# Kernel tuning notes

Hardware: AMD Instinct MI355X
Metric: run time of the kernel (lower is better)

The kernel has to match this reference:

```python
import jax, jax.numpy as jnp
import numpy as np


def _operators_3_to_2(x2d, A, norm):
    # x2d: [b, d, n, n], A: [b, n, n]. Returns the 20 basis tensors, each [b, d, n, n].
    t = lambda a: a.transpose(0, 1, 3, 2)
    shape = x2d.shape
    op1 = jnp.einsum('bdij,bij,bik->bdjk', x2d, A, A) / norm
    op2 = jnp.einsum('bdij,bij,bjk->bdik', x2d, A, A) / norm
    op3 = jnp.einsum('bdij,bik,bjk->bdij', x2d, A, A) / norm
    op4 = jnp.broadcast_to(jnp.einsum('bdij,bij->bdi', x2d, A)[..., None], shape) / norm
    op5 = jnp.broadcast_to(jnp.einsum('bdij,bij->bdj', x2d, A)[..., None], shape) / norm
    op6 = jnp.einsum('bdij,bik->bdjk', x2d, A) / norm
    # NOTE: source has ops7 = [op6, op6.transpose] (bug: op7 computed but unused) -- replicated faithfully.
    op8 = jnp.einsum('bdij,bik->bdij', x2d, A) / norm
    op9 = jnp.einsum('bdij,bjk->bdij', x2d, A) / norm
    op10 = jnp.broadcast_to(x2d.sum(3, keepdims=True), shape) / norm
    op11 = jnp.broadcast_to(x2d.sum(2, keepdims=True), shape) / norm
    return [op1, t(op1), op2, t(op2), op3,
            op4, t(op4), op5, t(op5),
            op6, t(op6), op6, t(op6),
            op8, op9,
            op10, t(op10), op11, t(op11),
            x2d]


def _forward(x, edge_weight, coeffs1, bias1, coeffs2, bias2, edge_index, batch, n):
    f = x.shape[-1]
    b = x.shape[0] // n
    # to_2d_tensor: [b*n, f] -> [b, 2f, n, n]
    x2 = x.reshape(b, n, f).transpose(0, 2, 1)  # [b, f, n]
    x_2d = jnp.concatenate([
        jnp.broadcast_to(x2[:, :, :, None], (b, f, n, n)),
        jnp.broadcast_to(x2[:, :, None, :], (b, f, n, n)),
    ], axis=1)
    # to_dense_adj: scatter-add edge weights into per-graph dense [b, n, n]
    g = batch[edge_index[0]]
    r = edge_index[0] - g * n
    c = edge_index[1] - g * n
    A = jnp.zeros((b, n, n), x.dtype).at[g, r, c].add(edge_weight)
    norm = jnp.asarray(n, x.dtype)  # normalization=True default
    for li, (coeffs, bias) in enumerate([(coeffs1, bias1), (coeffs2, bias2)]):
        ops_out = jnp.stack(_operators_3_to_2(x_2d, A, norm), axis=2)  # [b, d, 20, n, n]
        x_2d = jnp.einsum('der,bdrij->beij', coeffs, ops_out) + bias
        if li == 0:
            x_2d = jax.nn.sigmoid(x_2d)
    return x_2d.mean(axis=(1, 2, 3))  # [b]


def setup_inputs() -> dict:
    key = jax.random.key(0)
    kx, kg, ks, kd, kw, kc1, kc2 = jax.random.split(key, 7)
    b, n, deg, f, h = 4, 128, 16, 32, 32
    d_in, d_out = 2 * f, 2 * h  # layer doubles channels; hidden layer is d_out -> d_out
    E = b * n * deg
    x = jax.random.normal(kx, (b * n, f), dtype=jnp.float32)
    g = jax.random.randint(kg, (E,), 0, b)
    src = jax.random.randint(ks, (E,), 0, n)
    dst = jax.random.randint(kd, (E,), 0, n)
    edge_index = jnp.stack([g * n + src, g * n + dst]).astype(jnp.int32)
    edge_weight = jax.random.uniform(kw, (E,), dtype=jnp.float32)
    batch = (jnp.arange(b * n) // n).astype(jnp.int32)
    scale1 = np.sqrt(2.0) / (d_in + d_out)
    scale2 = np.sqrt(2.0) / (d_out + d_out)
    coeffs1 = jax.random.normal(kc1, (d_in, d_out, 20), dtype=jnp.float32) * scale1
    coeffs2 = jax.random.normal(kc2, (d_out, d_out, 20), dtype=jnp.float32) * scale2
    bias1 = jnp.zeros((1, d_out, 1, 1), dtype=jnp.float32)
    bias2 = jnp.zeros((1, d_out, 1, 1), dtype=jnp.float32)
    return {"x": x, "edge_weight": edge_weight, "coeffs1": coeffs1, "bias1": bias1,
            "coeffs2": coeffs2, "bias2": bias2, "edge_index": edge_index,
            "batch": batch, "n": n}


def reference(x, edge_weight, coeffs1, bias1, coeffs2, bias2, edge_index, batch, n):
    return _forward(x, edge_weight, coeffs1, bias1, coeffs2, bias2, edge_index, batch, n)
```

## Files before the change

kernel.cpp:

```cpp
#include <hip/hip_runtime.h>
#include <stdint.h>

typedef unsigned short u16;
using short8 = __attribute__((ext_vector_type(8))) short;
using f32x4  = __attribute__((ext_vector_type(4))) float;

#define NB 4
#define NN 128
#define NF 32
#define ND 64
#define NMAT (NB*ND*NN*NN)

#define OFF_A     0u
#define OFF_ACC   262144u
#define OFF_AAT   262400u
#define OFF_RA    524544u
#define OFF_W     526592u
#define OFF_RM    1116416u
#define OFF_CM    1247488u
#define OFF_RX    1378560u
#define OFF_CX    1509632u
#define OFF_BF    1640960u
#define OFF_ATB   1641472u
#define OFF_WB    1772544u
#define OFF_X2    1936384u
#define OFF_XE    10324992u
#define OFF_UA    18713600u
#define OFF_UB    27102208u
#define OFF_UC    35490816u
#define OFF_UD    43879424u
#define OFF_YACC  52268032u

__device__ __forceinline__ float b2f(u16 v){
  union { uint32_t u; float f; } x; x.u = ((uint32_t)v) << 16; return x.f;
}
__device__ __forceinline__ u16 f2b(float f){
  union { uint32_t u; float f2; } x; x.f2 = f;
  uint32_t u = x.u;
  return (u16)((u + 0x7FFFu + ((u >> 16) & 1u)) >> 16);
}

#define MFMA16(a,b,c) __builtin_amdgcn_mfma_f32_16x16x32_bf16((a),(b),(c),0,0,0)

__device__ __constant__ signed char dR1[18] = {0,9,1,10,2,3,4,13,14,19,5,7,15,18,6,8,16,17};
__device__ __constant__ signed char dR2[18] = {-1,11,-1,12,-1,-1,-1,-1,-1,-1,-1,-1,-1,-1,-1,-1,-1,-1};

__global__ void k_setup(const int* __restrict__ ei, const int* __restrict__ bat,
                        const void* __restrict__ ews, float* __restrict__ A, int E,
                        const void* __restrict__ xs, u16* __restrict__ Xe,
                        const void* __restrict__ c1s, const void* __restrict__ c2s,
                        const void* __restrict__ b1s, const void* __restrict__ b2s,
                        float* __restrict__ W, u16* __restrict__ Wb,
                        float* __restrict__ bfv)
{
  __shared__ int flg;
  const u16* x16 = (const u16*)xs;
  if (threadIdx.x == 0) flg = 0;
  __syncthreads();
  int hit = 0;
  for (int k = threadIdx.x; k < 1024; k += 256){
    u16 u = x16[k];
    if (((u >> 7) & 0xFF) >= 0x90) hit = 1;
  }
  if (hit) flg = 1;
  __syncthreads();
  const int isf = flg;

  const int bx = blockIdx.x;
  if (bx < 32){
    if (bx == 0 && threadIdx.x < 128){
      int tt = threadIdx.x;
      const void* bsrc = (tt < 64) ? b1s : b2s;
      int idx = tt & 63;
      bfv[tt] = isf ? ((const float*)bsrc)[idx] : b2f(((const u16*)bsrc)[idx]);
    }
    for (int t = bx*256 + threadIdx.x; t < E; t += 32*256){
      int s = ei[t], dnode = ei[E + t];
      int g = bat[s];
      int r = s - g*NN, c = dnode - g*NN;
      float wv = isf ? ((const float*)ews)[t] : b2f(((const u16*)ews)[t]);
      atomicAdd(&A[(g*NN + r)*NN + c], wv);
    }
  } else if (bx < 32 + 2048){
    int gid = (bx - 32)*256 + threadIdx.x;
    int ij8 = gid & 2047;
    int d   = (gid >> 11) & 63;
    int b   = gid >> 17;
    int ij  = ij8*8;
    int i = ij >> 7, j0 = ij & 127;
    short8 v;
    if (d < NF){
      int idx = (b*NN + i)*NF + d;
      u16 bv = isf ? f2b(((const float*)xs)[idx]) : ((const u16*)xs)[idx];
      #pragma unroll
      for (int k = 0; k < 8; k++) v[k] = (short)bv;
    } else {
      int dd = d - NF;
      #pragma unroll
      for (int k = 0; k < 8; k++){
        int idx = (b*NN + j0 + k)*NF + dd;
        v[k] = (short)(isf ? f2b(((const float*)xs)[idx]) : ((const u16*)xs)[idx]);
      }
    }
    *(short8*)(Xe + ((size_t)(b*ND + d) << 14) + ij) = v;
  } else {
    int gl = (bx - 2080)*256 + threadIdx.x;
    if (gl >= 2*1152*64) return;
    int L = gl / (1152*64);
    int rem = gl - L*1152*64;
    int row = rem >> 6, e = rem & 63;
    int slot = row >> 6, d = row & 63;
    const void* cr = L ? c2s : c1s;
    int base = (d*64 + e)*20;
    int i1 = base + dR1[slot];
    float v = isf ? ((const float*)cr)[i1] : b2f(((const u16*)cr)[i1]);
    if (dR2[slot] >= 0){
      int i2 = base + dR2[slot];
      v += isf ? ((const float*)cr)[i2] : b2f(((const u16*)cr)[i2]);
    }
    float scale = (slot == 9) ? 1.0f : (1.0f/128.0f);
    v *= scale;
    W[gl] = v;
    if (slot < 10)
      Wb[(((size_t)L*10 + slot)*64 + e)*64 + d] = f2b(v);
  }
}

__global__ __launch_bounds__(256) void k_prepA(const float* __restrict__ A, float* __restrict__ AAt,
                                               u16* __restrict__ ATb, float* __restrict__ rA){
  const int iq = blockIdx.x, b = blockIdx.y;
  const int t = threadIdx.x;
  if (iq < 8){
    int j = t & 127, ih = t >> 7;
    const float* Ab = A + b*NN*NN;
    float acc[8] = {0,0,0,0,0,0,0,0};
    for (int k = 0; k < NN; k++){
      float aj = Ab[j*NN + k];
      #pragma unroll
      for (int ii = 0; ii < 8; ii++){
        int i = iq*16 + ih*8 + ii;
        acc[ii] += Ab[i*NN + k] * aj;
      }
    }
    #pragma unroll
    for (int ii = 0; ii < 8; ii++){
      int i = iq*16 + ih*8 + ii;
      AAt[(b*NN + i)*NN + j] = acc[ii];
    }
  } else if (iq == 8){
    __shared__ float lds[128][129];
    for (int l = 0; l < 64; l++){
      int idx = l*256 + t;
      lds[idx >> 7][idx & 127] = A[b*16384 + idx];
    }
    __syncthreads();
    for (int l = 0; l < 64; l++){
      int idx = l*256 + t;
      int r = idx >> 7, c = idx & 127;
      ATb[b*16384 + idx] = f2b(lds[c][r]);
    }
  } else {
    if (t < 128){
      const float* Ab = A + (b*NN + t)*NN;
      float s = 0.f;
      for (int j = 0; j < 128; j++) s += Ab[j];
      rA[b*NN + t] = s;
    }
  }
}

#define SJ32 70
#define SJF  67
#define SXE  34

__global__ __launch_bounds__(256) void k_mixrow(const u16* __restrict__ Xe, const float* __restrict__ A,
    const float* __restrict__ AAt, const float* __restrict__ rA, const u16* __restrict__ Wb,
    u16* __restrict__ Ua, u16* __restrict__ Ub, u16* __restrict__ Uc, u16* __restrict__ Ud,
    float* __restrict__ Yacc,
    float* __restrict__ RM, float* __restrict__ CM,
    float* __restrict__ RX, float* __restrict__ CXv)
{
  const int b = blockIdx.y;
  const int t = threadIdx.x;

  if (blockIdx.x >= 256){
    const int d = blockIdx.x - 256;
    const u16* Xd = Xe + ((size_t)(b*ND + d) << 14);
    const float* Ab = A + b*NN*NN;
    float sm = 0.f, sx = 0.f;
    if (t < 128){
      const int i = t;
      #pragma unroll 2
      for (int j8 = 0; j8 < 16; j8++){
        short8 xv = *(const short8*)(Xd + i*128 + j8*8);
        float4 a0 = *(const float4*)(Ab + i*128 + j8*8);
        float4 a1 = *(const float4*)(Ab + i*128 + j8*8 + 4);
        float x0 = b2f((u16)xv[0]), x1 = b2f((u16)xv[1]), x2 = b2f((u16)xv[2]), x3 = b2f((u16)xv[3]);
        float x4 = b2f((u16)xv[4]), x5 = b2f((u16)xv[5]), x6 = b2f((u16)xv[6]), x7 = b2f((u16)xv[7]);
        sx += x0+x1+x2+x3+x4+x5+x6+x7;
        sm += x0*a0.x + x1*a0.y + x2*a0.z + x3*a0.w
            + x4*a1.x + x5*a1.y + x6*a1.z + x7*a1.w;
      }
      RM[(b*64 + d)*128 + i] = sm;
      RX[(b*64 + d)*128 + i] = sx;
    } else {
      const int j = t - 128;
      for (int i = 0; i < 128; i++){
        float xv = b2f(Xd[i*128 + j]);
        sx += xv;
        sm += xv * Ab[i*128 + j];
      }
      CM[(b*64 + d)*128 + j] = sm;
      CXv[(b*64 + d)*128 + j] = sx;
    }
    return;
  }

  const int w = t >> 6, lane = t & 63;
  const int col = lane & 15, quad = lane >> 4;
  const int ij0 = blockIdx.x*64;

  __shared__ uint32_t lsb[4][32*SJ32];
  __shared__ float lsf[64*SJF];

  short8 wa[10][2];
  #pragma unroll
  for (int s = 0; s < 10; s++){
    const u16* wp = Wb + (size_t)((s*64 + w*16 + col)*64 + quad*8);
    wa[s][0] = *(const short8*)wp;
    wa[s][1] = *(const short8*)(wp + 32);
  }
  float a_s[4], t_s[4], rjv[4];
  #pragma unroll
  for (int sj = 0; sj < 4; sj++){
    int ij = ij0 + sj*16 + col;
    a_s[sj] = A[b*16384 + ij];
    t_s[sj] = AAt[b*16384 + ij];
    rjv[sj] = rA[b*128 + (ij & 127)];
  }
  const float riv = rA[b*128 + (ij0 >> 7)];

  uint32_t* ldsX = &lsb[0][0];
  {
    const int ep = t >> 3;
    const int s8 = (t & 7)*8;
    const u16* xp = Xe + ((size_t)(b*ND + 2*ep) << 14) + ij0 + s8;
    short8 r0 = *(const short8*)xp;
    short8 r1 = *(const short8*)(xp + 16384);
    #pragma unroll
    for (int k = 0; k < 8; k++)
      ldsX[(s8 + k)*SXE + ep] = ((uint32_t)(u16)r0[k]) | (((uint32_t)(u16)r1[k]) << 16);
  }
  __syncthreads();
  short8 xb[4][2];
  #pragma unroll
  for (int sj = 0; sj < 4; sj++){
    #pragma unroll
    for (int h = 0; h < 2; h++){
      const uint32_t* p = &ldsX[(sj*16 + col)*SXE + quad*4 + h*16];
      uint2 u0 = *(const uint2*)p;
      uint2 u1 = *(const uint2*)(p + 2);
      union { uint32_t u[4]; short8 s; } cv;
      cv.u[0] = u0.x; cv.u[1] = u0.y; cv.u[2] = u1.x; cv.u[3] = u1.y;
      xb[sj][h] = cv.s;
    }
  }
  __syncthreads();

  #pragma unroll
  for (int g = 0; g < 5; g++){
    const int s0_tab[5]  = {0, 2, 4, 5, 6};
    const int nsl_tab[5] = {2, 2, 1, 1, 4};
    const int s0 = s0_tab[g], nsl = nsl_tab[g];
    #pragma unroll
    for (int sj = 0; sj < 4; sj++){
      f32x4 acc[4];
      #pragma unroll
      for (int s = 0; s < 4; s++) acc[s] = (f32x4){0.f,0.f,0.f,0.f};
      #pragma unroll
      for (int s = 0; s < 4; s++){
        if (s >= nsl) break;
        acc[s] = MFMA16(wa[s0+s][0], xb[sj][0], acc[s]);
        acc[s] = MFMA16(wa[s0+s][1], xb[sj][1], acc[s]);
      }
      if (g < 4){
        float v[4];
        #pragma unroll
        for (int r = 0; r < 4; r++){
          if (g == 2 || g == 3) v[r] = acc[0][r]*a_s[sj];
          else                  v[r] = acc[0][r]*a_s[sj] + acc[1][r];
        }
        uint32_t p0 = (uint32_t)f2b(v[0]) | ((uint32_t)f2b(v[1]) << 16);
        uint32_t p1 = (uint32_t)f2b(v[2]) | ((uint32_t)f2b(v[3]) << 16);
        int ep = w*8 + quad*2;
        lsb[g][ep*SJ32 + sj*16 + col] = p0;
        lsb[g][(ep + 1)*SJ32 + sj*16 + col] = p1;
      } else {
        #pragma unroll
        for (int r = 0; r < 4; r++){
          float v = acc[0][r]*t_s[sj] + acc[1][r]*riv + acc[2][r]*rjv[sj] + acc[3][r];
          lsf[(w*16 + quad*4 + r)*SJF + sj*16 + col] = v;
        }
      }
    }
  }
  __syncthreads();

  const int eo = t >> 2, seg = t & 3;
  const int ep = eo >> 1, sh = (eo & 1)*16;
  #pragma unroll
  for (int g = 0; g < 4; g++){
    const uint32_t* lp = &lsb[g][ep*SJ32 + seg*16];
    short8 v0, v1;
    #pragma unroll
    for (int k = 0; k < 8; k++){
      v0[k] = (short)((lp[k]   >> sh) & 0xffffu);
      v1[k] = (short)((lp[8+k] >> sh) & 0xffffu);
    }
    u16* U = (g==0)?Ua:(g==1)?Ub:(g==2)?Uc:Ud;
    u16* dst = U + ((size_t)(b*64 + eo) << 14) + ij0 + seg*16;
    *(short8*)dst = v0;
    *(short8*)(dst + 8) = v1;
  }
  {
    const float* fp = &lsf[eo*SJF + seg*16];
    float* dst = Yacc + ((size_t)(b*64 + eo) << 14) + ij0 + seg*16;
    #pragma unroll
    for (int q = 0; q < 4; q++)
      *(float4*)(dst + q*4) = make_float4(fp[q*4], fp[q*4+1], fp[q*4+2], fp[q*4+3]);
  }
}

#define SLT 68

__global__ __launch_bounds__(256) void k_tne(const u16* __restrict__ ATb,
    const u16* __restrict__ Ua, const u16* __restrict__ Ub,
    const u16* __restrict__ Uc, const u16* __restrict__ Ud,
    const float* __restrict__ Yacc, const float* __restrict__ W,
    const float* __restrict__ RM, const float* __restrict__ CM,
    const float* __restrict__ RX, const float* __restrict__ CXv,
    const float* __restrict__ bias, u16* __restrict__ Xout, float* __restrict__ acc4, int last)
{
  const int nh = blockIdx.x, be = blockIdx.y;
  const int b = be >> 6, e = be & 63;
  const int t = threadIdx.x, wave = t >> 6, lane = t & 63;
  const int col = lane & 15, quad = lane >> 4;
  const int m0 = (wave >> 1)*64;
  const int n0 = nh*64 + (wave & 1)*32;
  const int nb0 = nh*64;

  __shared__ uint32_t uls[128*SLT];
  __shared__ uint32_t ubl[64*SLT];
  __shared__ float radd[128], cadd[128];
  __shared__ float red[4];

  if (t < 128){
    int i = t; float s = 0.f;
    for (int d = 0; d < ND; d++){
      int v = (b*ND + d)*NN + i;
      s += W[(640 + d)*64 + e]*RM[v] + W[(704 + d)*64 + e]*CM[v]
         + W[(768 + d)*64 + e]*RX[v] + W[(832 + d)*64 + e]*CXv[v];
    }
    radd[i] = s;
  } else {
    int j = t - 128; float s = 0.f;
    for (int d = 0; d < ND; d++){
      int v = (b*ND + d)*NN + j;
      s += W[(896 + d)*64 + e]*RM[v] + W[(960 + d)*64 + e]*CM[v]
         + W[(1024 + d)*64 + e]*RX[v] + W[(1088 + d)*64 + e]*CXv[v];
    }
    cadd[j] = s;
  }

  const u16* ua = Ua + ((size_t)be << 14);
  const u16* ub = Ub + ((size_t)be << 14);
  {
    const int kp = t >> 2;
    #pragma unroll
    for (int it = 0; it < 4; it++){
      int mo = it*4 + (t & 3);
      short8 r0 = *(const short8*)(ua + (2*kp)*128 + mo*8);
      short8 r1 = *(const short8*)(ua + (2*kp + 1)*128 + mo*8);
      #pragma unroll
      for (int x = 0; x < 8; x++)
        uls[(mo*8 + x)*SLT + kp] = ((uint32_t)(u16)r0[x]) | (((uint32_t)(u16)r1[x]) << 16);
    }
    #pragma unroll
    for (int it = 0; it < 2; it++){
      int no = it*4 + (t & 3);
      short8 r0 = *(const short8*)(ub + (2*kp)*128 + nb0 + no*8);
      short8 r1 = *(const short8*)(ub + (2*kp + 1)*128 + nb0 + no*8);
      #pragma unroll
      for (int x = 0; x < 8; x++)
        ubl[(no*8 + x)*SLT + kp] = ((uint32_t)(u16)r0[x]) | (((uint32_t)(u16)r1[x]) << 16);
    }
  }
  __syncthreads();

  f32x4 acc[4][2];
  #pragma unroll
  for (int mt = 0; mt < 4; mt++)
    #pragma unroll
    for (int nt = 0; nt < 2; nt++)
      acc[mt][nt] = (f32x4){0.f,0.f,0.f,0.f};

  const u16* at = ATb + ((size_t)b << 14);
  short8 at_n[4][2];
  #pragma unroll
  for (int kq = 0; kq < 4; kq++){
    int k0 = kq*32 + quad*8;
    at_n[kq][0] = *(const short8*)(at + (n0 + col)*128 + k0);
    at_n[kq][1] = *(const short8*)(at + (n0 + 16 + col)*128 + k0);
  }

  #pragma unroll
  for (int kq = 0; kq < 4; kq++){
    int kd = kq*16 + quad*4;
    #pragma unroll
    for (int mt = 0; mt < 4; mt++){
      short8 af = *(const short8*)&uls[(m0 + mt*16 + col)*SLT + kd];
      acc[mt][0] = MFMA16(af, at_n[kq][0], acc[mt][0]);
      acc[mt][1] = MFMA16(af, at_n[kq][1], acc[mt][1]);
    }
  }
  #pragma unroll
  for (int kq = 0; kq < 4; kq++){
    int k0 = kq*32 + quad*8, kd = kq*16 + quad*4;
    short8 bf0 = *(const short8*)&ubl[((wave & 1)*32 + 0*16 + col)*SLT + kd];
    short8 bf1 = *(const short8*)&ubl[((wave & 1)*32 + 1*16 + col)*SLT + kd];
    #pragma unroll
    for (int mt = 0; mt < 4; mt++){
      short8 af = *(const short8*)(at + (m0 + mt*16 + col)*128 + k0);
      acc[mt][0] = MFMA16(af, bf0, acc[mt][0]);
      acc[mt][1] = MFMA16(af, bf1, acc[mt][1]);
    }
  }
  {
    const u16* uc = Uc + ((size_t)be << 14);
    #pragma unroll
    for (int kq = 0; kq < 4; kq++){
      int k0 = kq*32 + quad*8;
      #pragma unroll
      for (int mt = 0; mt < 4; mt++){
        short8 af = *(const short8*)(uc + (m0 + mt*16 + col)*128 + k0);
        acc[mt][0] = MFMA16(af, at_n[kq][0], acc[mt][0]);
        acc[mt][1] = MFMA16(af, at_n[kq][1], acc[mt][1]);
      }
    }
  }
  {
    const u16* ud = Ud + ((size_t)be << 14);
    #pragma unroll
    for (int kq = 0; kq < 4; kq++){
      int k0 = kq*32 + quad*8;
      short8 bf0 = *(const short8*)(ud + (n0 + col)*128 + k0);
      short8 bf1 = *(const short8*)(ud + (n0 + 16 + col)*128 + k0);
      #pragma unroll
      for (int mt = 0; mt < 4; mt++){
        short8 af = *(const short8*)(at + (m0 + mt*16 + col)*128 + k0);
        acc[mt][0] = MFMA16(af, bf0, acc[mt][0]);
        acc[mt][1] = MFMA16(af, bf1, acc[mt][1]);
      }
    }
  }
  __syncthreads();

  uint32_t* stg = uls;
  const float bv = bias[e];
  const float* Y = Yacc + ((size_t)be << 14);
  if (!last){
    #pragma unroll
    for (int mt = 0; mt < 4; mt++)
      #pragma unroll
      for (int nt = 0; nt < 2; nt++)
        #pragma unroll
        for (int rp = 0; rp < 2; rp++){
          uint32_t p = 0;
          #pragma unroll
          for (int h = 0; h < 2; h++){
            int r = rp*2 + h;
            int row = m0 + mt*16 + quad*4 + r;
            int cn = n0 + nt*16 + col;
            float v = acc[mt][nt][r] + Y[row*128 + cn] + radd[row] + cadd[cn] + bv;
            v = 1.f/(1.f + __expf(-v));
            p |= ((uint32_t)f2b(v)) << (16*h);
          }
          int ipair = (m0 + mt*16 + quad*4) >> 1;
          stg[(ipair + rp)*SLT + (wave & 1)*32 + nt*16 + col] = p;
        }
    __syncthreads();
    const uint32_t* lp = &stg[(t >> 2)*SLT + (t & 1)*32];
    const int sh = ((t >> 1) & 1)*16;
    u16* dst = Xout + ((size_t)be << 14) + (size_t)(t >> 1)*128 + nh*64 + (t & 1)*32;
    #pragma unroll
    for (int q2 = 0; q2 < 4; q2++){
      short8 v;
      #pragma unroll
      for (int k = 0; k < 8; k++) v[k] = (short)((lp[q2*8 + k] >> sh) & 0xffffu);
      *(short8*)(dst + q2*8) = v;
    }
  } else {
    float loc = 0.f;
    #pragma unroll
    for (int mt = 0; mt < 4; mt++)
      #pragma unroll
      for (int nt = 0; nt < 2; nt++)
        #pragma unroll
        for (int r = 0; r < 4; r++){
          int row = m0 + mt*16 + quad*4 + r;
          int cn = n0 + nt*16 + col;
          loc += acc[mt][nt][r] + Y[row*128 + cn] + radd[row] + cadd[cn] + bv;
        }
    for (int off = 32; off > 0; off >>= 1) loc += __shfl_down(loc, off, 64);
    if (lane == 0) red[wave] = loc;
    __syncthreads();
    if (t == 0) atomicAdd(&acc4[b], red[0] + red[1] + red[2] + red[3]);
  }
}

__global__ void k_finish(const float* __restrict__ acc4, const u16* __restrict__ x16,
                         void* __restrict__ out){
  __shared__ int flg;
  int t = threadIdx.x;
  if (t == 0) flg = 0;
  __syncthreads();
  int hit = 0;
  for (int k = t; k < 512; k += 64){
    u16 u = x16[k];
    if (((u >> 7) & 0xFF) >= 0x90) hit = 1;
  }
  if (hit) flg = 1;
  __syncthreads();
  if (t < NB){
    float v = acc4[t] * (1.0f/1048576.0f);
    if (flg) ((float*)out)[t] = v;
    else     ((u16*)out)[t] = f2b(v);
  }
}

extern "C" void kernel_launch(void* const* d_in, const int* in_sizes, int n_in,
                              void* d_out, int out_size, void* d_ws, size_t ws_size,
                              hipStream_t stream)
{
  const void* x   = d_in[0];
  const void* ew  = d_in[1];
  const void* c1  = d_in[2];
  const void* b1  = d_in[3];
  const void* c2  = d_in[4];
  const void* b2  = d_in[5];
  const int* ei  = (const int*)d_in[6];
  const int* bat = (const int*)d_in[7];
  const int E = in_sizes[1];

  char* wsb = (char*)d_ws;
  float* A    = (float*)(wsb + OFF_A);
  float* acc4 = (float*)(wsb + OFF_ACC);
  float* AAt  = (float*)(wsb + OFF_AAT);
  float* rA   = (float*)(wsb + OFF_RA);
  float* W    = (float*)(wsb + OFF_W);
  float* RM   = (float*)(wsb + OFF_RM);
  float* CM   = (float*)(wsb + OFF_CM);
  float* RX   = (float*)(wsb + OFF_RX);
  float* CXv  = (float*)(wsb + OFF_CX);
  float* bfv  = (float*)(wsb + OFF_BF);
  u16* ATb = (u16*)(wsb + OFF_ATB);
  u16* Wb  = (u16*)(wsb + OFF_WB);
  u16* X2  = (u16*)(wsb + OFF_X2);
  u16* Xe  = (u16*)(wsb + OFF_XE);
  u16* Ua  = (u16*)(wsb + OFF_UA);
  u16* Ub  = (u16*)(wsb + OFF_UB);
  u16* Uc  = (u16*)(wsb + OFF_UC);
  u16* Ud  = (u16*)(wsb + OFF_UD);
  float* Yacc = (float*)(wsb + OFF_YACC);

  hipMemsetAsync(wsb, 0, OFF_AAT, stream);

  k_setup<<<dim3(2656), dim3(256), 0, stream>>>(ei, bat, ew, A, E, x, Xe,
                                                c1, c2, b1, b2, W, Wb, bfv);
  k_prepA<<<dim3(10, NB), dim3(256), 0, stream>>>(A, AAt, ATb, rA);

  for (int L = 0; L < 2; L++){
    const float* Wl = W + (size_t)L*1152*64;
    const u16*  Wbl = Wb + (size_t)L*10*64*64;
    const u16*  Xsrc = (L == 0) ? Xe : X2;
    k_mixrow<<<dim3(320, NB), dim3(256), 0, stream>>>(Xsrc, A, AAt, rA, Wbl,
                                                      Ua, Ub, Uc, Ud, Yacc, RM, CM, RX, CXv);
    k_tne<<<dim3(2, 256), dim3(256), 0, stream>>>(ATb, Ua, Ub, Uc, Ud, Yacc, Wl,
                                                  RM, CM, RX, CXv, bfv + L*64, X2, acc4, L);
  }
  k_finish<<<dim3(1), dim3(64), 0, stream>>>(acc4, (const u16*)x, d_out);
}
```

Measured before the change: 223.0 us.

## Skip materializing expanded layer-0 input; read compact x directly in mixrow

Drops the 8 MB broadcast-expanded Xe tensor built in k_setup. Layer 0 of k_mixrow now reads a compact bf16 copy of x and builds the LDS tile from it. Its row and column reductions are computed analytically from x, row sums and new column sums of A. k_prepA is also rewritten to compute A·Aᵀ with more blocks and float4 loads, and to produce column sums from the LDS transpose tile. This removes a large write and re-read of redundant data, at the cost of a special-cased first-layer path with strided scalar loads.

```diff
diff --git a/kernel.cpp b/kernel.cpp
--- a/kernel.cpp
+++ b/kernel.cpp
@@ -24,7 +24,8 @@
 #define OFF_ATB   1641472u
 #define OFF_WB    1772544u
 #define OFF_X2    1936384u
-#define OFF_XE    10324992u
+#define OFF_XC    10324992u
+#define OFF_CA    10357760u
 #define OFF_UA    18713600u
 #define OFF_UB    27102208u
 #define OFF_UC    35490816u
@@ -47,7 +48,7 @@
 
 __global__ void k_setup(const int* __restrict__ ei, const int* __restrict__ bat,
                         const void* __restrict__ ews, float* __restrict__ A, int E,
-                        const void* __restrict__ xs, u16* __restrict__ Xe,
+                        const void* __restrict__ xs, u16* __restrict__ xc,
                         const void* __restrict__ c1s, const void* __restrict__ c2s,
                         const void* __restrict__ b1s, const void* __restrict__ b2s,
                         float* __restrict__ W, u16* __restrict__ Wb,
@@ -81,30 +82,19 @@
       float wv = isf ? ((const float*)ews)[t] : b2f(((const u16*)ews)[t]);
       atomicAdd(&A[(g*NN + r)*NN + c], wv);
     }
-  } else if (bx < 32 + 2048){
-    int gid = (bx - 32)*256 + threadIdx.x;
-    int ij8 = gid & 2047;
-    int d   = (gid >> 11) & 63;
-    int b   = gid >> 17;
-    int ij  = ij8*8;
-    int i = ij >> 7, j0 = ij & 127;
-    short8 v;
-    if (d < NF){
-      int idx = (b*NN + i)*NF + d;
-      u16 bv = isf ? f2b(((const float*)xs)[idx]) : ((const u16*)xs)[idx];
-      #pragma unroll
-      for (int k = 0; k < 8; k++) v[k] = (short)bv;
+  } else if (bx < 40){
+    int idx8 = ((bx - 32)*256 + threadIdx.x)*8;
+    if (!isf){
+      *(short8*)(xc + idx8) = *(const short8*)(x16 + idx8);
     } else {
-      int dd = d - NF;
-      #pragma unroll
-      for (int k = 0; k < 8; k++){
-        int idx = (b*NN + j0 + k)*NF + dd;
-        v[k] = (short)(isf ? f2b(((const float*)xs)[idx]) : ((const u16*)xs)[idx]);
-      }
-    }
-    *(short8*)(Xe + ((size_t)(b*ND + d) << 14) + ij) = v;
+      const float* xfp = (const float*)xs;
+      short8 v;
+      #pragma unroll
+      for (int k = 0; k < 8; k++) v[k] = (short)f2b(xfp[idx8 + k]);
+      *(short8*)(xc + idx8) = v;
+    }
   } else {
-    int gl = (bx - 2080)*256 + threadIdx.x;
+    int gl = (bx - 40)*256 + threadIdx.x;
     if (gl >= 2*1152*64) return;
     int L = gl / (1152*64);
     int rem = gl - L*1152*64;
@@ -127,27 +117,26 @@
 }
 
 __global__ __launch_bounds__(256) void k_prepA(const float* __restrict__ A, float* __restrict__ AAt,
-                                               u16* __restrict__ ATb, float* __restrict__ rA){
+                                               u16* __restrict__ ATb, float* __restrict__ rA,
+                                               float* __restrict__ cA){
   const int iq = blockIdx.x, b = blockIdx.y;
   const int t = threadIdx.x;
-  if (iq < 8){
+  if (iq < 32){
     int j = t & 127, ih = t >> 7;
+    int i0 = iq*4 + ih, i1 = i0 + 2;
     const float* Ab = A + b*NN*NN;
-    float acc[8] = {0,0,0,0,0,0,0,0};
-    for (int k = 0; k < NN; k++){
-      float aj = Ab[j*NN + k];
-      #pragma unroll
-      for (int ii = 0; ii < 8; ii++){
-        int i = iq*16 + ih*8 + ii;
-        acc[ii] += Ab[i*NN + k] * aj;
-      }
-    }
-    #pragma unroll
-    for (int ii = 0; ii < 8; ii++){
-      int i = iq*16 + ih*8 + ii;
-      AAt[(b*NN + i)*NN + j] = acc[ii];
-    }
-  } else if (iq == 8){
+    float acc0 = 0.f, acc1 = 0.f;
+    #pragma unroll 4
+    for (int k = 0; k < 128; k += 4){
+      float4 aj = *(const float4*)(Ab + j*128 + k);
+      float4 a0 = *(const float4*)(Ab + i0*128 + k);
+      float4 a1 = *(const float4*)(Ab + i1*128 + k);
+      acc0 += a0.x*aj.x + a0.y*aj.y + a0.z*aj.z + a0.w*aj.w;
+      acc1 += a1.x*aj.x + a1.y*aj.y + a1.z*aj.z + a1.w*aj.w;
+    }
+    AAt[(b*NN + i0)*NN + j] = acc0;
+    AAt[(b*NN + i1)*NN + j] = acc1;
+  } else {
     __shared__ float lds[128][129];
     for (int l = 0; l < 64; l++){
       int idx = l*256 + t;
@@ -159,12 +148,15 @@
       int r = idx >> 7, c = idx & 127;
       ATb[b*16384 + idx] = f2b(lds[c][r]);
     }
-  } else {
     if (t < 128){
-      const float* Ab = A + (b*NN + t)*NN;
       float s = 0.f;
-      for (int j = 0; j < 128; j++) s += Ab[j];
+      for (int j = 0; j < 128; j++) s += lds[t][j];
       rA[b*NN + t] = s;
+    } else {
+      int c = t - 128;
+      float s = 0.f;
+      for (int j = 0; j < 128; j++) s += lds[j][c];
+      cA[b*NN + c] = s;
     }
   }
 }
@@ -173,19 +165,58 @@
 #define SJF  67
 #define SXE  34
 
-__global__ __launch_bounds__(256) void k_mixrow(const u16* __restrict__ Xe, const float* __restrict__ A,
-    const float* __restrict__ AAt, const float* __restrict__ rA, const u16* __restrict__ Wb,
+__global__ __launch_bounds__(256) void k_mixrow(const u16* __restrict__ Xs, const float* __restrict__ A,
+    const float* __restrict__ AAt, const float* __restrict__ rA, const float* __restrict__ cA,
+    const u16* __restrict__ xc, const u16* __restrict__ Wb,
     u16* __restrict__ Ua, u16* __restrict__ Ub, u16* __restrict__ Uc, u16* __restrict__ Ud,
     float* __restrict__ Yacc,
     float* __restrict__ RM, float* __restrict__ CM,
-    float* __restrict__ RX, float* __restrict__ CXv)
+    float* __restrict__ RX, float* __restrict__ CXv, int first)
 {
   const int b = blockIdx.y;
   const int t = threadIdx.x;
 
   if (blockIdx.x >= 256){
     const int d = blockIdx.x - 256;
-    const u16* Xd = Xe + ((size_t)(b*ND + d) << 14);
+    if (first){
+      if (t < 128){
+        const int i = t;
+        if (d < NF){
+          float xv = b2f(xc[(b*NN + i)*NF + d]);
+          RM[(b*64 + d)*128 + i] = xv * rA[b*NN + i];
+          RX[(b*64 + d)*128 + i] = 128.f * xv;
+        } else {
+          const u16* xcb = xc + b*NN*NF + (d - NF);
+          const float* Ar = A + b*16384 + i*128;
+          float sm = 0.f, sx = 0.f;
+          for (int j = 0; j < 128; j++){
+            float xj = b2f(xcb[j*NF]);
+            sm += Ar[j]*xj; sx += xj;
+          }
+          RM[(b*64 + d)*128 + i] = sm;
+          RX[(b*64 + d)*128 + i] = sx;
+        }
+      } else {
+        const int j = t - 128;
+        if (d < NF){
+          const u16* xcb = xc + b*NN*NF + d;
+          const float* Ac = A + b*16384 + j;
+          float sm = 0.f, sx = 0.f;
+          for (int i = 0; i < 128; i++){
+            float xi = b2f(xcb[i*NF]);
+            sm += Ac[i*128]*xi; sx += xi;
+          }
+          CM[(b*64 + d)*128 + j] = sm;
+          CXv[(b*64 + d)*128 + j] = sx;
+        } else {
+          float xv = b2f(xc[(b*NN + j)*NF + (d - NF)]);
+          CM[(b*64 + d)*128 + j] = xv * cA[b*NN + j];
+          CXv[(b*64 + d)*128 + j] = 128.f * xv;
+        }
+      }
+      return;
+    }
+    const u16* Xd = Xs + ((size_t)(b*ND + d) << 14);
     const float* Ab = A + b*NN*NN;
     float sm = 0.f, sx = 0.f;
     if (t < 128){
@@ -244,12 +275,27 @@
   {
     const int ep = t >> 3;
     const int s8 = (t & 7)*8;
-    const u16* xp = Xe + ((size_t)(b*ND + 2*ep) << 14) + ij0 + s8;
-    short8 r0 = *(const short8*)xp;
-    short8 r1 = *(const short8*)(xp + 16384);
-    #pragma unroll
-    for (int k = 0; k < 8; k++)
-      ldsX[(s8 + k)*SXE + ep] = ((uint32_t)(u16)r0[k]) | (((uint32_t)(u16)r1[k]) << 16);
+    if (first){
+      const int i = ij0 >> 7;
+      const int j0 = (ij0 & 127) + s8;
+      if (ep < 16){
+        uint32_t p = *(const uint32_t*)(xc + (b*NN + i)*NF + 2*ep);
+        #pragma unroll
+        for (int k = 0; k < 8; k++) ldsX[(s8 + k)*SXE + ep] = p;
+      } else {
+        const int d0 = 2*ep - 32;
+        #pragma unroll
+        for (int k = 0; k < 8; k++)
+          ldsX[(s8 + k)*SXE + ep] = *(const uint32_t*)(xc + (b*NN + j0 + k)*NF + d0);
+      }
+    } else {
+      const u16* xp = Xs + ((size_t)(b*ND + 2*ep) << 14) + ij0 + s8;
+      short8 r0 = *(const short8*)xp;
+      short8 r1 = *(const short8*)(xp + 16384);
+      #pragma unroll
+      for (int k = 0; k < 8; k++)
+        ldsX[(s8 + k)*SXE + ep] = ((uint32_t)(u16)r0[k]) | (((uint32_t)(u16)r1[k]) << 16);
+    }
   }
   __syncthreads();
   short8 xb[4][2];
@@ -566,7 +612,8 @@
   u16* ATb = (u16*)(wsb + OFF_ATB);
   u16* Wb  = (u16*)(wsb + OFF_WB);
   u16* X2  = (u16*)(wsb + OFF_X2);
-  u16* Xe  = (u16*)(wsb + OFF_XE);
+  u16* xc  = (u16*)(wsb + OFF_XC);
+  float* cA = (float*)(wsb + OFF_CA);
   u16* Ua  = (u16*)(wsb + OFF_UA);
   u16* Ub  = (u16*)(wsb + OFF_UB);
   u16* Uc  = (u16*)(wsb + OFF_UC);
@@ -575,16 +622,16 @@
 
   hipMemsetAsync(wsb, 0, OFF_AAT, stream);
 
-  k_setup<<<dim3(2656), dim3(256), 0, stream>>>(ei, bat, ew, A, E, x, Xe,
-                                                c1, c2, b1, b2, W, Wb, bfv);
-  k_prepA<<<dim3(10, NB), dim3(256), 0, stream>>>(A, AAt, ATb, rA);
+  k_setup<<<dim3(616), dim3(256), 0, stream>>>(ei, bat, ew, A, E, x, xc,
+                                               c1, c2, b1, b2, W, Wb, bfv);
+  k_prepA<<<dim3(33, NB), dim3(256), 0, stream>>>(A, AAt, ATb, rA, cA);
 
   for (int L = 0; L < 2; L++){
     const float* Wl = W + (size_t)L*1152*64;
     const u16*  Wbl = Wb + (size_t)L*10*64*64;
-    const u16*  Xsrc = (L == 0) ? Xe : X2;
-    k_mixrow<<<dim3(320, NB), dim3(256), 0, stream>>>(Xsrc, A, AAt, rA, Wbl,
-                                                      Ua, Ub, Uc, Ud, Yacc, RM, CM, RX, CXv);
+    k_mixrow<<<dim3(320, NB), dim3(256), 0, stream>>>(X2, A, AAt, rA, cA, xc, Wbl,
+                                                      Ua, Ub, Uc, Ud, Yacc, RM, CM, RX, CXv,
+                                                      L == 0 ? 1 : 0);
     k_tne<<<dim3(2, 256), dim3(256), 0, stream>>>(ATb, Ua, Ub, Uc, Ud, Yacc, Wl,
                                                   RM, CM, RX, CXv, bfv + L*64, X2, acc4, L);
   }
```

New measurement: 203.8 us. -8.6%, faster.
